# Performance work log

Measured on AMD Instinct MI355X. Metric: run time of the kernel, lower is better.

The kernel has to match this reference:

```python
import jax, jax.numpy as jnp
import numpy as np

BETA = 0.5
ITERS = 20


def bjorck_orthonormalize(w, beta, iters):
    def body(w, _):
        wtw = jnp.matmul(w.T, w)            # [in, in]
        w = (1.0 + beta) * w - beta * jnp.matmul(w, wtw)
        return w, None
    w, _ = jax.lax.scan(body, w, None, length=iters)
    return w


def setup_inputs() -> dict:
    key = jax.random.key(0)
    k1, k2, k3 = jax.random.split(key, 3)
    x = jax.random.normal(k1, (4, 8192, 1024), dtype=jnp.float32)
    kernel = jax.random.normal(k2, (1024, 1024), dtype=jnp.float32)
    bias = jax.random.normal(k3, (1024,), dtype=jnp.float32)
    return {"x": x, "kernel": kernel, "bias": bias}


def reference(x, kernel, bias):
    # safe Bjorck scaling: sqrt(in_features * out_features)
    scaling = jnp.sqrt(jnp.asarray(kernel.shape[0] * kernel.shape[1], dtype=kernel.dtype))
    w = bjorck_orthonormalize(kernel / scaling, BETA, ITERS)  # [in, out]
    y = jnp.einsum('bsi,io->bso', x, w)
    y = y + bias.reshape((1, 1, -1))
    return y
```

## Files before the change

kernel.cpp:

```cpp
#include <hip/hip_runtime.h>
#include <cstdint>

typedef _Float16 half8 __attribute__((ext_vector_type(8)));
typedef _Float16 half4v __attribute__((ext_vector_type(4)));
typedef float f32x4 __attribute__((ext_vector_type(4)));

__device__ __forceinline__ void async_copy16(const void* g, void* l) {
    __builtin_amdgcn_global_load_lds((const __attribute__((address_space(1))) void*)g,
                                     (__attribute__((address_space(3))) void*)l, 16, 0, 0);
}

__global__ __launch_bounds__(256) void prep_w(const float* __restrict__ K,
                                              _Float16* __restrict__ w0,
                                              _Float16* __restrict__ w0T) {
    __shared__ float tile[64][65];
    const int t  = threadIdx.x;
    const int bi = blockIdx.y * 64;
    const int bj = blockIdx.x * 64;
    const int r0 = t >> 4;
    const int c4 = (t & 15) * 4;
#pragma unroll
    for (int rr = 0; rr < 4; ++rr) {
        int r = r0 + rr * 16;
        f32x4 v = *(const f32x4*)&K[(size_t)(bi + r) * 1024 + bj + c4];
        v *= 0.03125f;
        half4v h;
        h[0] = (_Float16)v[0]; h[1] = (_Float16)v[1];
        h[2] = (_Float16)v[2]; h[3] = (_Float16)v[3];
        *(half4v*)&w0[(size_t)(bi + r) * 1024 + bj + c4] = h;
        tile[r][c4 + 0] = v[0]; tile[r][c4 + 1] = v[1];
        tile[r][c4 + 2] = v[2]; tile[r][c4 + 3] = v[3];
    }
    __syncthreads();
    const int cT = t >> 4;
    const int rT = (t & 15) * 4;
#pragma unroll
    for (int cc = 0; cc < 4; ++cc) {
        int c = cT + cc * 16;
        half4v h;
        h[0] = (_Float16)tile[rT + 0][c]; h[1] = (_Float16)tile[rT + 1][c];
        h[2] = (_Float16)tile[rT + 2][c]; h[3] = (_Float16)tile[rT + 3][c];
        *(half4v*)&w0T[(size_t)(bj + c) * 1024 + bi + rT] = h;
    }
}

template <int EPI>
__global__ __launch_bounds__(512) void gemm1k(const _Float16* __restrict__ A,
                                              const _Float16* __restrict__ BT,
                                              const _Float16* __restrict__ wcur,
                                              _Float16* __restrict__ out,
                                              _Float16* __restrict__ outT) {
    __shared__ _Float16 sA[2][8192];
    __shared__ _Float16 sB[2][8192];
    const int t = threadIdx.x;
    const int b = blockIdx.x;
    const int xcd = b & 7, j = b >> 3;
    const int m0 = (((xcd & 1) << 3) + (j & 7)) << 6;
    const int n0 = (((xcd >> 1) << 2) + (j >> 3)) << 6;
    const int ln = t & 63, wv = t >> 6;
    const int wm = wv >> 1, wn = wv & 1;
    const int q  = ln >> 4, l15 = ln & 15;

    f32x4 acc[2];
#pragma unroll
    for (int jn = 0; jn < 2; ++jn) {
        acc[jn][0] = 0.f; acc[jn][1] = 0.f;
        acc[jn][2] = 0.f; acc[jn][3] = 0.f;
    }

    auto stage = [&](int buf, int k0) {
#pragma unroll
        for (int rnd = 0; rnd < 2; ++rnd) {
            int c = t + rnd * 512;
            int row = c >> 4, g = c & 15;
            int gs = g ^ (row & 15);
            async_copy16(A + (size_t)(m0 + row) * 1024 + k0 + gs * 8, &sA[buf][c * 8]);
            async_copy16(BT + (size_t)(n0 + row) * 1024 + k0 + gs * 8, &sB[buf][c * 8]);
        }
    };
    auto frag = [&](const _Float16* s, int row, int kc) -> half8 {
        return *(const half8*)&s[row * 128 + ((kc ^ (row & 15)) << 3)];
    };

    stage(0, 0);
    int cur = 0;
#pragma unroll 1
    for (int it = 0; it < 8; ++it) {
        __syncthreads();
        if (it < 7) stage(cur ^ 1, (it + 1) * 128);
#pragma unroll
        for (int kk = 0; kk < 4; ++kk) {
            half8 a0 = frag(sA[cur], wm * 16 + l15, kk * 4 + q);
            half8 b0 = frag(sB[cur], wn * 32 + 0  + l15, kk * 4 + q);
            half8 b1 = frag(sB[cur], wn * 32 + 16 + l15, kk * 4 + q);
            acc[0] = __builtin_amdgcn_mfma_f32_16x16x32_f16(a0, b0, acc[0], 0, 0, 0);
            acc[1] = __builtin_amdgcn_mfma_f32_16x16x32_f16(a0, b1, acc[1], 0, 0, 0);
        }
        cur ^= 1;
    }

    const int row0 = m0 + wm * 16 + q * 4;
#pragma unroll
    for (int jn = 0; jn < 2; ++jn) {
        int col = n0 + wn * 32 + jn * 16 + l15;
        if (EPI == 0) {
#pragma unroll
            for (int r = 0; r < 4; ++r)
                out[(size_t)(row0 + r) * 1024 + col] = (_Float16)acc[jn][r];
        } else {
            half4v hT;
#pragma unroll
            for (int r = 0; r < 4; ++r) {
                float w0v = (float)wcur[(size_t)(row0 + r) * 1024 + col];
                float nv  = 1.5f * w0v - 4.8828125e-4f * acc[jn][r];
                _Float16 h = (_Float16)nv;
                out[(size_t)(row0 + r) * 1024 + col] = h;
                hT[r] = h;
            }
            *(half4v*)&outT[(size_t)col * 1024 + row0] = hT;
        }
    }
}

__global__ __launch_bounds__(256) void gemm_big(const float* __restrict__ X,
                                                const _Float16* __restrict__ BT,
                                                const float* __restrict__ bias,
                                                float* __restrict__ Y) {
    __shared__ _Float16 sA[2][128 * 40];
    __shared__ _Float16 sB[2][128 * 32];
    const int t   = threadIdx.x;
    const int bb  = blockIdx.x;
    const int xcd = bb & 7;
    const int jj  = bb >> 3;
    const int rr  = jj >> 5;
    const int ss  = jj & 31;
    const int mt  = rr * 32 + xcd * 4 + (ss >> 3);
    const int nt  = ss & 7;
    const int m0 = mt * 128, n0 = nt * 128;
    const int ln = t & 63, wv = t >> 6;
    const int wm = wv >> 1, wn = wv & 1;
    const int q  = ln >> 4, l15 = ln & 15;

    f32x4 acc[4][4];
#pragma unroll
    for (int i = 0; i < 4; ++i)
#pragma unroll
        for (int j = 0; j < 4; ++j) {
            acc[i][j][0] = 0.f; acc[i][j][1] = 0.f;
            acc[i][j][2] = 0.f; acc[i][j][3] = 0.f;
        }

    auto loadA = [&](int k0, f32x4* va) {
#pragma unroll
        for (int rnd = 0; rnd < 4; ++rnd) {
            int c = t + rnd * 256;
            int row = c >> 3, s4 = c & 7;
            va[rnd] = *(const f32x4*)&X[(size_t)(m0 + row) * 1024 + k0 + s4 * 4];
        }
    };
    auto writeA = [&](int buf, const f32x4* va) {
#pragma unroll
        for (int rnd = 0; rnd < 4; ++rnd) {
            int c = t + rnd * 256;
            int row = c >> 3, s4 = c & 7;
            half4v h;
            h[0] = (_Float16)va[rnd][0]; h[1] = (_Float16)va[rnd][1];
            h[2] = (_Float16)va[rnd][2]; h[3] = (_Float16)va[rnd][3];
            *(half4v*)&sA[buf][row * 40 + s4 * 4] = h;
        }
    };
    auto stageB = [&](int buf, int k0) {
#pragma unroll
        for (int rnd = 0; rnd < 2; ++rnd) {
            int c = t + rnd * 256;
            int row = c >> 2, s = c & 3;
            int gs = s ^ ((row >> 1) & 3);
            async_copy16(BT + (size_t)(n0 + row) * 1024 + k0 + gs * 8, &sB[buf][c * 8]);
        }
    };

    f32x4 va[4];
    loadA(0, va);
    stageB(0, 0);
    writeA(0, va);
    int cur = 0;
#pragma unroll 1
    for (int it = 0; it < 32; ++it) {
        __syncthreads();
        if (it < 31) {
            loadA((it + 1) * 32, va);
            stageB(cur ^ 1, (it + 1) * 32);
        }
        half8 a[4], bfr[4];
#pragma unroll
        for (int im = 0; im < 4; ++im) {
            int row = wm * 64 + im * 16 + l15;
            a[im] = *(const half8*)&sA[cur][row * 40 + q * 8];
        }
#pragma unroll
        for (int jn = 0; jn < 4; ++jn) {
            int row = wn * 64 + jn * 16 + l15;
            bfr[jn] = *(const half8*)&sB[cur][row * 32 + ((q ^ ((row >> 1) & 3)) << 3)];
        }
#pragma unroll
        for (int im = 0; im < 4; ++im)
#pragma unroll
            for (int jn = 0; jn < 4; ++jn)
                acc[im][jn] = __builtin_amdgcn_mfma_f32_16x16x32_f16(a[im], bfr[jn], acc[im][jn], 0, 0, 0);
        if (it < 31) writeA(cur ^ 1, va);
        cur ^= 1;
    }

#pragma unroll
    for (int jn = 0; jn < 4; ++jn) {
        int col = n0 + wn * 64 + jn * 16 + l15;
        float bv = bias[col];
#pragma unroll
        for (int im = 0; im < 4; ++im) {
            int row0 = m0 + wm * 64 + im * 16 + q * 4;
#pragma unroll
            for (int r = 0; r < 4; ++r)
                Y[(size_t)(row0 + r) * 1024 + col] = acc[im][jn][r] * 0.03125f + bv;
        }
    }
}

extern "C" void kernel_launch(void* const* d_in, const int* in_sizes, int n_in,
                              void* d_out, int out_size, void* d_ws, size_t ws_size,
                              hipStream_t stream) {
    (void)in_sizes; (void)n_in; (void)out_size; (void)ws_size;
    const float* x    = (const float*)d_in[0];
    const float* kern = (const float*)d_in[1];
    const float* bias = (const float*)d_in[2];
    float* y = (float*)d_out;

    char* ws = (char*)d_ws;
    const size_t SZ = (size_t)1024 * 1024 * sizeof(_Float16);
    _Float16* wh[2] = {(_Float16*)(ws + 0 * SZ), (_Float16*)(ws + 1 * SZ)};
    _Float16* wT[2] = {(_Float16*)(ws + 2 * SZ), (_Float16*)(ws + 3 * SZ)};
    _Float16* Sh    = (_Float16*)(ws + 4 * SZ);

    prep_w<<<dim3(16, 16), 256, 0, stream>>>(kern, wh[0], wT[0]);

    for (int it = 0; it < 20; ++it) {
        int c = it & 1, n = c ^ 1;
        gemm1k<0><<<256, 512, 0, stream>>>(wT[c], wT[c], nullptr, Sh, nullptr);
        gemm1k<1><<<256, 512, 0, stream>>>(wh[c], Sh, wh[c], wh[n], wT[n]);
    }
    gemm_big<<<2048, 256, 0, stream>>>(x, wT[0], bias, y);
}
```

Baseline: 764.6 us.

## Deepen async copy pipelines to three stages with explicit vmcnt waits

Both the 1024x1024 Bjorck GEMM and the large activation GEMM move from double to triple-buffered shared-memory staging. Barriers are replaced by inline s_waitcnt vmcnt(N) plus s_barrier so that loads for two tiles ahead stay in flight while the current tile is computed. In the big GEMM, A register loads alternate between two register sets. The small GEMM also prefetches the epilogue's wcur values before the main loop. The cost is more LDS and registers, and hand-counted vmcnt values that must match the number of outstanding loads.

Measured after the change: 750.3 us. Within noise of the previous version (-1.9%).

```diff
diff --git a/kernel.cpp b/kernel.cpp
--- a/kernel.cpp
+++ b/kernel.cpp
@@ -50,8 +50,8 @@
                                               const _Float16* __restrict__ wcur,
                                               _Float16* __restrict__ out,
                                               _Float16* __restrict__ outT) {
-    __shared__ _Float16 sA[2][8192];
-    __shared__ _Float16 sB[2][8192];
+    __shared__ _Float16 sA[3][8192];
+    __shared__ _Float16 sB[3][8192];
     const int t = threadIdx.x;
     const int b = blockIdx.x;
     const int xcd = b & 7, j = b >> 3;
@@ -60,6 +60,18 @@
     const int ln = t & 63, wv = t >> 6;
     const int wm = wv >> 1, wn = wv & 1;
     const int q  = ln >> 4, l15 = ln & 15;
+    const int row0 = m0 + wm * 16 + q * 4;
+
+    float wpre[2][4];
+    if (EPI == 1) {
+#pragma unroll
+        for (int jn = 0; jn < 2; ++jn) {
+            int col = n0 + wn * 32 + jn * 16 + l15;
+#pragma unroll
+            for (int r = 0; r < 4; ++r)
+                wpre[jn][r] = (float)wcur[(size_t)(row0 + r) * 1024 + col];
+        }
+    }
 
     f32x4 acc[2];
 #pragma unroll
@@ -81,25 +93,28 @@
     auto frag = [&](const _Float16* s, int row, int kc) -> half8 {
         return *(const half8*)&s[row * 128 + ((kc ^ (row & 15)) << 3)];
     };
-
-    stage(0, 0);
-    int cur = 0;
-#pragma unroll 1
-    for (int it = 0; it < 8; ++it) {
-        __syncthreads();
-        if (it < 7) stage(cur ^ 1, (it + 1) * 128);
+    auto dostep = [&](int buf) {
 #pragma unroll
         for (int kk = 0; kk < 4; ++kk) {
-            half8 a0 = frag(sA[cur], wm * 16 + l15, kk * 4 + q);
-            half8 b0 = frag(sB[cur], wn * 32 + 0  + l15, kk * 4 + q);
-            half8 b1 = frag(sB[cur], wn * 32 + 16 + l15, kk * 4 + q);
+            half8 a0 = frag(sA[buf], wm * 16 + l15, kk * 4 + q);
+            half8 b0 = frag(sB[buf], wn * 32 + 0  + l15, kk * 4 + q);
+            half8 b1 = frag(sB[buf], wn * 32 + 16 + l15, kk * 4 + q);
             acc[0] = __builtin_amdgcn_mfma_f32_16x16x32_f16(a0, b0, acc[0], 0, 0, 0);
             acc[1] = __builtin_amdgcn_mfma_f32_16x16x32_f16(a0, b1, acc[1], 0, 0, 0);
         }
-        cur ^= 1;
-    }
-
-    const int row0 = m0 + wm * 16 + q * 4;
+    };
+
+    stage(0, 0);
+    stage(1, 128);
+#pragma unroll 1
+    for (int it = 0; it < 7; ++it) {
+        asm volatile("s_waitcnt vmcnt(4)\n\ts_barrier" ::: "memory");
+        if (it < 6) stage((it + 2) % 3, (it + 2) * 128);
+        dostep(it % 3);
+    }
+    asm volatile("s_waitcnt vmcnt(0)\n\ts_barrier" ::: "memory");
+    dostep(1);
+
 #pragma unroll
     for (int jn = 0; jn < 2; ++jn) {
         int col = n0 + wn * 32 + jn * 16 + l15;
@@ -111,8 +126,7 @@
             half4v hT;
 #pragma unroll
             for (int r = 0; r < 4; ++r) {
-                float w0v = (float)wcur[(size_t)(row0 + r) * 1024 + col];
-                float nv  = 1.5f * w0v - 4.8828125e-4f * acc[jn][r];
+                float nv  = 1.5f * wpre[jn][r] - 4.8828125e-4f * acc[jn][r];
                 _Float16 h = (_Float16)nv;
                 out[(size_t)(row0 + r) * 1024 + col] = h;
                 hT[r] = h;
@@ -127,7 +141,7 @@
                                                 const float* __restrict__ bias,
                                                 float* __restrict__ Y) {
     __shared__ _Float16 sA[2][128 * 40];
-    __shared__ _Float16 sB[2][128 * 32];
+    __shared__ _Float16 sB[3][128 * 32];
     const int t   = threadIdx.x;
     const int bb  = blockIdx.x;
     const int xcd = bb & 7;
@@ -178,38 +192,53 @@
             async_copy16(BT + (size_t)(n0 + row) * 1024 + k0 + gs * 8, &sB[buf][c * 8]);
         }
     };
-
-    f32x4 va[4];
-    loadA(0, va);
-    stageB(0, 0);
-    writeA(0, va);
-    int cur = 0;
-#pragma unroll 1
-    for (int it = 0; it < 32; ++it) {
-        __syncthreads();
-        if (it < 31) {
-            loadA((it + 1) * 32, va);
-            stageB(cur ^ 1, (it + 1) * 32);
-        }
+    auto compute = [&](int t_) {
         half8 a[4], bfr[4];
 #pragma unroll
         for (int im = 0; im < 4; ++im) {
             int row = wm * 64 + im * 16 + l15;
-            a[im] = *(const half8*)&sA[cur][row * 40 + q * 8];
+            a[im] = *(const half8*)&sA[t_ & 1][row * 40 + q * 8];
         }
 #pragma unroll
         for (int jn = 0; jn < 4; ++jn) {
             int row = wn * 64 + jn * 16 + l15;
-            bfr[jn] = *(const half8*)&sB[cur][row * 32 + ((q ^ ((row >> 1) & 3)) << 3)];
+            bfr[jn] = *(const half8*)&sB[t_ % 3][row * 32 + ((q ^ ((row >> 1) & 3)) << 3)];
         }
 #pragma unroll
         for (int im = 0; im < 4; ++im)
 #pragma unroll
             for (int jn = 0; jn < 4; ++jn)
                 acc[im][jn] = __builtin_amdgcn_mfma_f32_16x16x32_f16(a[im], bfr[jn], acc[im][jn], 0, 0, 0);
-        if (it < 31) writeA(cur ^ 1, va);
-        cur ^= 1;
-    }
+    };
+
+    f32x4 vaA[4], vaB[4];
+    loadA(0, vaA);
+    stageB(0, 0);
+    writeA(0, vaA);
+    loadA(32, vaB);
+    stageB(1, 32);
+
+#define BODY(T, VLD, VWR)                                                     \
+    {                                                                         \
+        asm volatile("s_waitcnt vmcnt(6) lgkmcnt(0)\n\ts_barrier" ::: "memory"); \
+        if ((T) + 2 < 32) {                                                   \
+            loadA(((T) + 2) * 32, VLD);                                       \
+            stageB(((T) + 2) % 3, ((T) + 2) * 32);                            \
+        }                                                                     \
+        compute(T);                                                           \
+        writeA(((T) + 1) & 1, VWR);                                           \
+    }
+
+#pragma unroll 1
+    for (int tp = 0; tp < 15; ++tp) {
+        int te = tp * 2;
+        BODY(te, vaA, vaB);
+        BODY(te + 1, vaB, vaA);
+    }
+    BODY(30, vaA, vaB);
+#undef BODY
+    asm volatile("s_waitcnt vmcnt(0) lgkmcnt(0)\n\ts_barrier" ::: "memory");
+    compute(31);
 
 #pragma unroll
     for (int jn = 0; jn < 4; ++jn) {
```
